# Kernel tuning notes

Measured on AMD Instinct MI355X. Metric: run time of the kernel, lower is better.

The kernel has to match this reference:

```python
import jax, jax.numpy as jnp
import numpy as np

N_NODES = 20000
N_EDGES = 320000
H = 4        # heads
C = 64       # channels per head
D = H * C    # 256, also input_dim
L = 4        # num_layers
NEG_SLOPE = 0.2


def setup_inputs() -> dict:
    key = jax.random.key(0)
    ks = jax.random.split(key, 8)
    x = jax.random.normal(ks[0], (N_NODES, D), jnp.float32)
    edge_index = jax.random.randint(ks[1], (2, N_EDGES), 0, N_NODES, dtype=jnp.int64)
    Ws = jax.random.normal(ks[2], (L, D, D), jnp.float32) * 0.05
    att_src = jax.random.normal(ks[3], (L, H, C), jnp.float32) * 0.05
    att_dst = jax.random.normal(ks[4], (L, H, C), jnp.float32) * 0.05
    biases = jax.random.normal(ks[5], (L, D), jnp.float32) * 0.05
    Wout = jax.random.normal(ks[6], (D, D), jnp.float32) * 0.05
    bout = jax.random.normal(ks[7], (D,), jnp.float32) * 0.05
    return {"x": x, "edge_index": edge_index, "Ws": Ws, "att_src": att_src,
            "att_dst": att_dst, "biases": biases, "Wout": Wout, "bout": bout}


def reference(x, edge_index, Ws, att_src, att_dst, biases, Wout, bout):
    n = x.shape[0]
    # PyG GATConv adds self-loops by default; same edge set each layer.
    loops = jnp.arange(n, dtype=edge_index.dtype)
    src = jnp.concatenate([edge_index[0], loops])  # message sources
    dst = jnp.concatenate([edge_index[1], loops])  # message targets (softmax groups)
    h = x
    for l in range(L):
        hp = (h @ Ws[l]).reshape(n, H, C)                      # [N,H,C]
        a_s = jnp.einsum('nhc,hc->nh', hp, att_src[l])          # [N,H]
        a_d = jnp.einsum('nhc,hc->nh', hp, att_dst[l])          # [N,H]
        e = jax.nn.leaky_relu(a_s[src] + a_d[dst], NEG_SLOPE)   # [E',H]
        # per-destination segment softmax (every node has a self-loop -> non-empty)
        m = jax.ops.segment_max(e, dst, num_segments=n)         # [N,H]
        ex = jnp.exp(e - m[dst])
        denom = jax.ops.segment_sum(ex, dst, num_segments=n)    # [N,H]
        alpha = ex / denom[dst]                                 # [E',H]
        msg = hp[src] * alpha[:, :, None]                       # [E',H,C]
        h = jax.ops.segment_sum(msg, dst, num_segments=n).reshape(n, D) + biases[l]
        h = jax.nn.elu(h)  # dropout is identity in eval mode
    g = jnp.mean(h, axis=0, keepdims=True)                      # mean pooling, single graph
    return g @ Wout + bout                                      # [1, D]
```

## Files before the change

### kernel.cpp

```cpp
#include <hip/hip_runtime.h>
#include <hip/hip_bf16.h>

#define H 4
#define C 64
#define D 256
#define NEG_SLOPE 0.2f
#define ESHIFT 8.0f

typedef _Float16 half_t;
typedef __attribute__((ext_vector_type(8))) _Float16 half8v;
typedef __attribute__((ext_vector_type(4))) float f32x4;


__device__ inline void fma_mix_pair(float& clo, float& chi, unsigned wu, float a) {
    asm("v_fma_mix_f32 %0, %2, %3, %0 op_sel_hi:[1,0,0]\n\t"
        "v_fma_mix_f32 %1, %2, %3, %1 op_sel:[1,0,0] op_sel_hi:[1,0,0]"
        : "+v"(clo), "+v"(chi)
        : "v"(wu), "v"(a));
}

__global__ void count_kernel(const int* __restrict__ ei, int E, int N, int* __restrict__ counts) {
    int i = blockIdx.x * blockDim.x + threadIdx.x;
    if (i >= E + N) return;
    int d = (i < E) ? ei[E + i] : (i - E);
    atomicAdd(&counts[d], 1);
}

__global__ __launch_bounds__(1024) void scan1(const int* __restrict__ counts,
                                              int* __restrict__ row_ptr,
                                              int* __restrict__ bsum, int N) {
    __shared__ int wsum[16];
    int tid = threadIdx.x, lane = tid & 63, wid = tid >> 6;
    int idx = blockIdx.x * 1024 + tid;
    int v = (idx < N) ? counts[idx] : 0;
    int val = v;
    #pragma unroll
    for (int o = 1; o < 64; o <<= 1) {
        int t = __shfl_up(val, o);
        if (lane >= o) val += t;
    }
    if (lane == 63) wsum[wid] = val;
    __syncthreads();
    int woff = 0;
    #pragma unroll
    for (int w = 0; w < 16; w++) woff += (w < wid) ? wsum[w] : 0;
    if (idx < N) row_ptr[idx] = woff + val - v;
    if (tid == 1023) bsum[blockIdx.x] = woff + val;
}

__global__ void scan2(int* __restrict__ bsum, int* __restrict__ row_ptr, int nb, int N) {
    int lane = threadIdx.x;
    int v = (lane < nb) ? bsum[lane] : 0;
    int val = v;
    #pragma unroll
    for (int o = 1; o < 64; o <<= 1) {
        int t = __shfl_up(val, o);
        if (lane >= o) val += t;
    }
    if (lane < nb) bsum[lane] = val - v;
    if (lane == 63) row_ptr[N] = val;
}

__global__ __launch_bounds__(1024) void scan3(int* __restrict__ row_ptr,
                                              const int* __restrict__ bsum,
                                              int* __restrict__ cursor, int N) {
    int idx = blockIdx.x * 1024 + threadIdx.x;
    if (idx >= N) return;
    int r = row_ptr[idx] + bsum[blockIdx.x];
    row_ptr[idx] = r;
    cursor[idx] = r;
}

__global__ void scatter_kernel(const int* __restrict__ ei, int E, int N,
                               int* __restrict__ cursor, int* __restrict__ csr_src) {
    int i = blockIdx.x * blockDim.x + threadIdx.x;
    if (i >= E + N) return;
    int s, d;
    if (i < E) { s = ei[i]; d = ei[E + i]; }
    else       { s = d = i - E; }
    int pos = atomicAdd(&cursor[d], 1);
    csr_src[pos] = s;
}

__global__ void conv_x(const float* __restrict__ in, half_t* __restrict__ xt, int total) {
    int t = blockIdx.x * blockDim.x + threadIdx.x;
    if (t >= total) return;
    int i = t >> 5, o = t & 31;
    const float* src = in + (size_t)i * 256 + o * 8;
    float4 v0 = *(const float4*)src;
    float4 v1 = *(const float4*)(src + 4);
    half_t q[8] __attribute__((aligned(16)));
    q[0] = (half_t)v0.x; q[1] = (half_t)v0.y; q[2] = (half_t)v0.z; q[3] = (half_t)v0.w;
    q[4] = (half_t)v1.x; q[5] = (half_t)v1.y; q[6] = (half_t)v1.z; q[7] = (half_t)v1.w;
    size_t dst = (size_t)(i >> 4) * 4096 + (o >> 2) * 512 + (o & 3) * 128 + (i & 15) * 8;
    *(half8v*)(xt + dst) = *(half8v*)q;
}

__global__ void conv_w(const float* __restrict__ W, half_t* __restrict__ wt, int total) {
    int idx = blockIdx.x * blockDim.x + threadIdx.x;
    if (idx >= total) return;
    int Lr = idx & 63;
    int s  = (idx >> 6) & 7;
    int cb = (idx >> 9) & 3;
    int h  = (idx >> 11) & 3;
    int l  = idx >> 13;
    int col = h * 64 + cb * 16 + (Lr & 15);
    int k0  = 32 * s + (Lr >> 4) * 8;
    half_t q[8] __attribute__((aligned(16)));
    #pragma unroll
    for (int j = 0; j < 8; j++)
        q[j] = (half_t)W[(size_t)l * 65536 + (size_t)(k0 + j) * 256 + col];
    *(half8v*)(wt + (size_t)idx * 8) = *(half8v*)q;
}

__global__ __launch_bounds__(256) void gemm_f16(
    const half_t* __restrict__ At, const half_t* __restrict__ Wt,
    const float* __restrict__ asrc, const float* __restrict__ adst,
    half_t* __restrict__ hp, float* __restrict__ as_out, float* __restrict__ ad_out,
    int Npad) {
    __shared__ float sp[4][4][16], sd[4][4][16];
    int nwg = gridDim.x;
    int bq = nwg >> 3, br = nwg & 7;
    int xcd = blockIdx.x & 7, bidx = blockIdx.x >> 3;
    int swz = (xcd < br ? xcd * (bq + 1) : br * (bq + 1) + (xcd - br) * bq) + bidx;
    int cb = threadIdx.x >> 6, lane = threadIdx.x & 63;
    int h = swz & 3, pg = swz >> 2;
    int rlo = lane & 15, q = lane >> 4;
    const half_t* pb = Wt + (size_t)h * 16384 + (size_t)cb * 4096 + lane * 8;

    half8v B[8];
    #pragma unroll
    for (int s = 0; s < 8; s++) B[s] = *(const half8v*)(pb + s * 512);

    float av = asrc[h * 64 + cb * 16 + rlo];
    float dv = adst[h * 64 + cb * 16 + rlo];
    half_t* hph = hp + (size_t)h * Npad * 64;

    #pragma unroll
    for (int pp = 0; pp < 4; pp++) {
        int p = pg * 4 + pp;
        const half_t* pa = At + (size_t)p * 4096 + lane * 8;

        f32x4 acc = (f32x4){0.f, 0.f, 0.f, 0.f};
        half8v A0 = *(const half8v*)(pa);
        half8v A1;
        #pragma unroll
        for (int s = 0; s < 8; s += 2) {
            A1 = *(const half8v*)(pa + (s + 1) * 512);
            acc = __builtin_amdgcn_mfma_f32_16x16x32_f16(A0, B[s], acc, 0, 0, 0);
            if (s < 6) A0 = *(const half8v*)(pa + (s + 2) * 512);
            acc = __builtin_amdgcn_mfma_f32_16x16x32_f16(A1, B[s + 1], acc, 0, 0, 0);
        }

        int grow = p * 16 + q * 4;
        #pragma unroll
        for (int i = 0; i < 4; i++)
            hph[(size_t)(grow + i) * 64 + cb * 16 + rlo] = (half_t)acc[i];

        float ps[4], pd[4];
        #pragma unroll
        for (int i = 0; i < 4; i++) { ps[i] = acc[i] * av; pd[i] = acc[i] * dv; }
        #pragma unroll
        for (int mask = 1; mask <= 8; mask <<= 1) {
            #pragma unroll
            for (int i = 0; i < 4; i++) {
                ps[i] += __shfl_xor(ps[i], mask);
                pd[i] += __shfl_xor(pd[i], mask);
            }
        }
        if (rlo == 0) {
            #pragma unroll
            for (int i = 0; i < 4; i++) {
                sp[pp][cb][q * 4 + i] = ps[i];
                sd[pp][cb][q * 4 + i] = pd[i];
            }
        }
    }
    __syncthreads();
    if (threadIdx.x < 64) {
        int pp = threadIdx.x >> 4, r = threadIdx.x & 15;
        float s_ = sp[pp][0][r] + sp[pp][1][r] + sp[pp][2][r] + sp[pp][3][r];
        float d_ = sd[pp][0][r] + sd[pp][1][r] + sd[pp][2][r] + sd[pp][3][r];
        int grow = (pg * 4 + pp) * 16 + r;
        as_out[(size_t)grow * 4 + h] = s_;
        ad_out[(size_t)grow * 4 + h] = d_;
    }
}

#define AGG_BODY(g)                                                          \
    {                                                                        \
        int e_ = 2 * (g) + es;                                               \
        int s_ = __float_as_int(pk[wv][e_][0]);                              \
        float a_ = pk[wv][e_][4 + hh];                                       \
        const uint4 w_ = *(const uint4*)(hpb + (size_t)s_ * 64);             \
        asum += a_;                                                          \
        fma_mix_pair(c0, c1, w_.x, a_);                                      \
        fma_mix_pair(c2, c3, w_.y, a_);                                      \
        fma_mix_pair(c4, c5, w_.z, a_);                                      \
        fma_mix_pair(c6, c7, w_.w, a_);                                      \
    }

__global__ __launch_bounds__(256) void gat_aggregate(
    const half_t* __restrict__ hp, const float* __restrict__ as_, const float* __restrict__ ad_,
    const int* __restrict__ row_ptr, const int* __restrict__ csr_src,
    const float* __restrict__ bias, half_t* __restrict__ hnext, int N, int Npad) {
    __shared__ float pk[4][64][8];
    int wv = threadIdx.x >> 6, lane = threadIdx.x & 63;
    int d = blockIdx.x * 4 + wv;
    if (d >= N) return;
    int r0 = row_ptr[d], deg = row_ptr[d + 1] - r0;
    float4 adv = *(const float4*)&ad_[(size_t)d * 4];

    if (deg <= 64) {
        if (lane < deg) {
            int s = csr_src[r0 + lane];
            float4 as4 = *(const float4*)&as_[(size_t)s * 4];
            float e0 = as4.x + adv.x, e1 = as4.y + adv.y;
            float e2 = as4.z + adv.z, e3 = as4.w + adv.w;
            e0 = e0 > 0.f ? e0 : NEG_SLOPE * e0;
            e1 = e1 > 0.f ? e1 : NEG_SLOPE * e1;
            e2 = e2 > 0.f ? e2 : NEG_SLOPE * e2;
            e3 = e3 > 0.f ? e3 : NEG_SLOPE * e3;
            float4 ex;
            ex.x = __expf(e0 - ESHIFT);
            ex.y = __expf(e1 - ESHIFT);
            ex.z = __expf(e2 - ESHIFT);
            ex.w = __expf(e3 - ESHIFT);
            pk[wv][lane][0] = __int_as_float(s);
            *(float4*)&pk[wv][lane][4] = ex;
        }

        int hh = lane >> 4;
        int es = (lane >> 3) & 1;
        int chq = lane & 7;
        const half_t* hpb = hp + (size_t)hh * Npad * 64 + chq * 8;
        float c0 = 0.f, c1 = 0.f, c2 = 0.f, c3 = 0.f;
        float c4 = 0.f, c5 = 0.f, c6 = 0.f, c7 = 0.f;
        float asum = 0.f;
        int full = deg >> 1;
        int g = 0;
        for (; g + 8 <= full; g += 8) {
            AGG_BODY(g)     AGG_BODY(g + 1) AGG_BODY(g + 2) AGG_BODY(g + 3)
            AGG_BODY(g + 4) AGG_BODY(g + 5) AGG_BODY(g + 6) AGG_BODY(g + 7)
        }
        for (; g + 4 <= full; g += 4) {
            AGG_BODY(g) AGG_BODY(g + 1) AGG_BODY(g + 2) AGG_BODY(g + 3)
        }
        for (; g < full; g++) { AGG_BODY(g) }
        if ((deg & 1) && es == 0) {
            int e_ = deg - 1;
            int s_ = __float_as_int(pk[wv][e_][0]);
            float a_ = pk[wv][e_][4 + hh];
            const uint4 w_ = *(const uint4*)(hpb + (size_t)s_ * 64);
            asum += a_;
            fma_mix_pair(c0, c1, w_.x, a_);
            fma_mix_pair(c2, c3, w_.y, a_);
            fma_mix_pair(c4, c5, w_.z, a_);
            fma_mix_pair(c6, c7, w_.w, a_);
        }
        c0 += __shfl_xor(c0, 8); c1 += __shfl_xor(c1, 8);
        c2 += __shfl_xor(c2, 8); c3 += __shfl_xor(c3, 8);
        c4 += __shfl_xor(c4, 8); c5 += __shfl_xor(c5, 8);
        c6 += __shfl_xor(c6, 8); c7 += __shfl_xor(c7, 8);
        asum += __shfl_xor(asum, 8);
        if (!(lane & 8)) {
            float inv = 1.0f / asum;
            int o = hh * 8 + chq;
            const float* bp = bias + o * 8;
            float vv[8] = {c0, c1, c2, c3, c4, c5, c6, c7};
            half_t oh[8] __attribute__((aligned(16)));
            #pragma unroll
            for (int j = 0; j < 8; j++) {
                float v = vv[j] * inv + bp[j];
                v = v > 0.f ? v : (__expf(v) - 1.0f);
                oh[j] = (half_t)v;
            }
            size_t dst = (size_t)(d >> 4) * 4096 + (o >> 2) * 512 + (o & 3) * 128 + (d & 15) * 8;
            *(half8v*)(hnext + dst) = *(half8v*)oh;
        }
    } else {
        float advA[4] = {adv.x, adv.y, adv.z, adv.w};
        #pragma unroll
        for (int hh = 0; hh < 4; hh++) {
            float advh = advA[hh];
            float ssum = 0.f;
            for (int i = lane; i < deg; i += 64) {
                int s = csr_src[r0 + i];
                float e = as_[(size_t)s * 4 + hh] + advh;
                e = e > 0.f ? e : NEG_SLOPE * e;
                ssum += __expf(e - ESHIFT);
            }
            #pragma unroll
            for (int o = 32; o; o >>= 1) ssum += __shfl_xor(ssum, o);
            float inv = 1.0f / ssum;
            const half_t* hph = hp + (size_t)hh * Npad * 64;
            float acc = 0.f;
            for (int i = 0; i < deg; i++) {
                int s = csr_src[r0 + i];
                float e = as_[(size_t)s * 4 + hh] + advh;
                e = e > 0.f ? e : NEG_SLOPE * e;
                acc += __expf(e - ESHIFT) * (float)hph[(size_t)s * 64 + lane];
            }
            float v = acc * inv + bias[hh * 64 + lane];
            v = v > 0.f ? v : (__expf(v) - 1.0f);
            int c = hh * 64 + lane;
            size_t dst = (size_t)(d >> 4) * 4096 + (c >> 5) * 512 + ((c >> 3) & 3) * 128 + (d & 15) * 8 + (c & 7);
            hnext[dst] = (half_t)v;
        }
    }
}

__global__ __launch_bounds__(256) void col_sum_f16(const half_t* __restrict__ hin,
                                                   float* __restrict__ partial, int N, int rows_per_blk) {
    int c = threadIdx.x;
    int r0 = blockIdx.x * rows_per_blk;
    int r1 = min(r0 + rows_per_blk, N);
    int coff = (c >> 5) * 512 + ((c >> 3) & 3) * 128 + (c & 7);
    float acc = 0.f;
    for (int r = r0; r < r1; r++)
        acc += (float)hin[(size_t)(r >> 4) * 4096 + coff + (r & 15) * 8];
    partial[(size_t)blockIdx.x * 256 + c] = acc;
}

__global__ __launch_bounds__(256) void final_kernel(const float* __restrict__ partial,
                                                    const float* __restrict__ Wout,
                                                    const float* __restrict__ bout,
                                                    float* __restrict__ out, float invN, int nb) {
    __shared__ float gl[256];
    int j = threadIdx.x;
    float s = 0.f;
    for (int b = 0; b < nb; b++) s += partial[(size_t)b * 256 + j];
    gl[j] = s;
    __syncthreads();
    float acc = 0.f;
    for (int i = 0; i < 256; i++) acc += gl[i] * Wout[i * 256 + j];
    out[j] = acc * invN + bout[j];
}

extern "C" void kernel_launch(void* const* d_in, const int* in_sizes, int n_in,
                              void* d_out, int out_size, void* d_ws, size_t ws_size,
                              hipStream_t stream) {
    const float* x       = (const float*)d_in[0];
    const int*   ei      = (const int*)d_in[1];
    const float* Ws      = (const float*)d_in[2];
    const float* att_src = (const float*)d_in[3];
    const float* att_dst = (const float*)d_in[4];
    const float* biases  = (const float*)d_in[5];
    const float* Wout    = (const float*)d_in[6];
    const float* bout    = (const float*)d_in[7];
    float* out = (float*)d_out;

    int N = in_sizes[0] / D;
    int E = in_sizes[1] / 2;
    int L = in_sizes[2] / (D * D);
    int Etot = E + N;
    int Npad = (N + 63) & ~63;

    char* ws = (char*)d_ws;
    size_t off = 0;
    auto alloc = [&](size_t bytes) -> void* {
        void* p = ws + off;
        off = (off + bytes + 255) & ~(size_t)255;
        return p;
    };
    half_t* xt     = (half_t*)alloc((size_t)Npad * D * 2);
    half_t* hp     = (half_t*)alloc((size_t)Npad * D * 2);
    float* a_s     = (float*)alloc((size_t)Npad * H * 4);
    float* a_d     = (float*)alloc((size_t)Npad * H * 4);
    half_t* wt     = (half_t*)alloc((size_t)L * D * D * 2);
    int*   counts  = (int*)alloc((size_t)N * 4);
    int*   row_ptr = (int*)alloc((size_t)(N + 1) * 4);
    int*   cursor  = (int*)alloc((size_t)N * 4);
    int*   bsum    = (int*)alloc(64 * 4);
    int*   csr_src = (int*)alloc((size_t)Etot * 4);
    int rows_per_blk = 254;
    int nb_pool = (N + rows_per_blk - 1) / rows_per_blk;
    float* partial = (float*)alloc((size_t)nb_pool * 256 * 4);
    if (off > ws_size) return;

    int thr = 256;

    int xtot = N * 32;
    conv_x<<<(xtot + thr - 1) / thr, thr, 0, stream>>>(x, xt, xtot);
    int wtot = L * 4 * 4 * 8 * 64;
    conv_w<<<(wtot + thr - 1) / thr, thr, 0, stream>>>(Ws, wt, wtot);

    hipMemsetAsync(counts, 0, (size_t)N * 4, stream);
    count_kernel<<<(Etot + thr - 1) / thr, thr, 0, stream>>>(ei, E, N, counts);
    int nb_scan = (N + 1023) / 1024;
    scan1<<<nb_scan, 1024, 0, stream>>>(counts, row_ptr, bsum, N);
    scan2<<<1, 64, 0, stream>>>(bsum, row_ptr, nb_scan, N);
    scan3<<<nb_scan, 1024, 0, stream>>>(row_ptr, bsum, cursor, N);
    scatter_kernel<<<(Etot + thr - 1) / thr, thr, 0, stream>>>(ei, E, N, cursor, csr_src);

    int gemm_blocks = (Npad / 64) * 4;
    int agg_blocks = (N + 3) / 4;
    for (int l = 0; l < L; l++) {
        gemm_f16<<<gemm_blocks, 256, 0, stream>>>(
            xt, wt + (size_t)l * D * D,
            att_src + (size_t)l * H * C, att_dst + (size_t)l * H * C,
            hp, a_s, a_d, Npad);
        gat_aggregate<<<agg_blocks, 256, 0, stream>>>(
            hp, a_s, a_d, row_ptr, csr_src, biases + (size_t)l * D, xt, N, Npad);
    }

    col_sum_f16<<<nb_pool, thr, 0, stream>>>(xt, partial, N, rows_per_blk);
    final_kernel<<<1, thr, 0, stream>>>(partial, Wout, bout, out, 1.0f / (float)N, nb_pool);
}
```

Baseline: 272.1 us.

## Split GAT aggregation by head with four destination nodes per wave

The aggregation grid now runs head-major. Each block covers one head and 16 destinations, and each wave handles 4 destinations using 16 lanes apiece, instead of one destination per wave across all 4 heads. The aim is to keep each head's slice of hp resident in L2 while its blocks run, and to shrink shared-memory staging to a 48-edge per-node buffer. The high-degree fallback is rewritten as a single fused pass with packed half loads. In exchange, edge indices and logits are re-read once per head, and lanes within a wave can diverge when the four nodes have different degrees.

```diff
diff --git a/kernel.cpp b/kernel.cpp
--- a/kernel.cpp
+++ b/kernel.cpp
@@ -6,6 +6,7 @@
 #define D 256
 #define NEG_SLOPE 0.2f
 #define ESHIFT 8.0f
+#define AGGC 48
 
 typedef _Float16 half_t;
 typedef __attribute__((ext_vector_type(8))) _Float16 half8v;
@@ -190,8 +191,8 @@
 #define AGG_BODY(g)                                                          \
     {                                                                        \
         int e_ = 2 * (g) + es;                                               \
-        int s_ = __float_as_int(pk[wv][e_][0]);                              \
-        float a_ = pk[wv][e_][4 + hh];                                       \
+        int s_ = __float_as_int(pk[wv][nn][e_][0]);                          \
+        float a_ = pk[wv][nn][e_][1];                                        \
         const uint4 w_ = *(const uint4*)(hpb + (size_t)s_ * 64);             \
         asum += a_;                                                          \
         fma_mix_pair(c0, c1, w_.x, a_);                                      \
@@ -203,54 +204,47 @@
 __global__ __launch_bounds__(256) void gat_aggregate(
     const half_t* __restrict__ hp, const float* __restrict__ as_, const float* __restrict__ ad_,
     const int* __restrict__ row_ptr, const int* __restrict__ csr_src,
-    const float* __restrict__ bias, half_t* __restrict__ hnext, int N, int Npad) {
-    __shared__ float pk[4][64][8];
+    const float* __restrict__ bias, half_t* __restrict__ hnext,
+    int N, int Npad, int ngroups) {
+    __shared__ float pk[4][4][AGGC][2];
     int wv = threadIdx.x >> 6, lane = threadIdx.x & 63;
-    int d = blockIdx.x * 4 + wv;
+    int h = blockIdx.x / ngroups;
+    int db = (blockIdx.x % ngroups) * 16;
+    int nn = lane >> 4;
+    int d = db + wv * 4 + nn;
     if (d >= N) return;
     int r0 = row_ptr[d], deg = row_ptr[d + 1] - r0;
-    float4 adv = *(const float4*)&ad_[(size_t)d * 4];
-
-    if (deg <= 64) {
-        if (lane < deg) {
-            int s = csr_src[r0 + lane];
-            float4 as4 = *(const float4*)&as_[(size_t)s * 4];
-            float e0 = as4.x + adv.x, e1 = as4.y + adv.y;
-            float e2 = as4.z + adv.z, e3 = as4.w + adv.w;
-            e0 = e0 > 0.f ? e0 : NEG_SLOPE * e0;
-            e1 = e1 > 0.f ? e1 : NEG_SLOPE * e1;
-            e2 = e2 > 0.f ? e2 : NEG_SLOPE * e2;
-            e3 = e3 > 0.f ? e3 : NEG_SLOPE * e3;
-            float4 ex;
-            ex.x = __expf(e0 - ESHIFT);
-            ex.y = __expf(e1 - ESHIFT);
-            ex.z = __expf(e2 - ESHIFT);
-            ex.w = __expf(e3 - ESHIFT);
-            pk[wv][lane][0] = __int_as_float(s);
-            *(float4*)&pk[wv][lane][4] = ex;
-        }
-
-        int hh = lane >> 4;
-        int es = (lane >> 3) & 1;
-        int chq = lane & 7;
-        const half_t* hpb = hp + (size_t)hh * Npad * 64 + chq * 8;
+    float adv = ad_[(size_t)d * 4 + h];
+    const half_t* hph = hp + (size_t)h * Npad * 64;
+
+    if (deg <= AGGC) {
+        int le = lane & 15;
+        #pragma unroll
+        for (int k = 0; k < 3; k++) {
+            int e = k * 16 + le;
+            if (e < deg) {
+                int s = csr_src[r0 + e];
+                float ev = as_[(size_t)s * 4 + h] + adv;
+                ev = ev > 0.f ? ev : NEG_SLOPE * ev;
+                pk[wv][nn][e][0] = __int_as_float(s);
+                pk[wv][nn][e][1] = __expf(ev - ESHIFT);
+            }
+        }
+        int es = (lane >> 3) & 1, chq = lane & 7;
+        const half_t* hpb = hph + chq * 8;
         float c0 = 0.f, c1 = 0.f, c2 = 0.f, c3 = 0.f;
         float c4 = 0.f, c5 = 0.f, c6 = 0.f, c7 = 0.f;
         float asum = 0.f;
         int full = deg >> 1;
         int g = 0;
-        for (; g + 8 <= full; g += 8) {
-            AGG_BODY(g)     AGG_BODY(g + 1) AGG_BODY(g + 2) AGG_BODY(g + 3)
-            AGG_BODY(g + 4) AGG_BODY(g + 5) AGG_BODY(g + 6) AGG_BODY(g + 7)
-        }
         for (; g + 4 <= full; g += 4) {
             AGG_BODY(g) AGG_BODY(g + 1) AGG_BODY(g + 2) AGG_BODY(g + 3)
         }
         for (; g < full; g++) { AGG_BODY(g) }
         if ((deg & 1) && es == 0) {
             int e_ = deg - 1;
-            int s_ = __float_as_int(pk[wv][e_][0]);
-            float a_ = pk[wv][e_][4 + hh];
+            int s_ = __float_as_int(pk[wv][nn][e_][0]);
+            float a_ = pk[wv][nn][e_][1];
             const uint4 w_ = *(const uint4*)(hpb + (size_t)s_ * 64);
             asum += a_;
             fma_mix_pair(c0, c1, w_.x, a_);
@@ -263,10 +257,10 @@
         c4 += __shfl_xor(c4, 8); c5 += __shfl_xor(c5, 8);
         c6 += __shfl_xor(c6, 8); c7 += __shfl_xor(c7, 8);
         asum += __shfl_xor(asum, 8);
-        if (!(lane & 8)) {
+        if (es == 0) {
             float inv = 1.0f / asum;
-            int o = hh * 8 + chq;
-            const float* bp = bias + o * 8;
+            int o = h * 8 + chq;
+            const float* bp = bias + h * 64 + chq * 8;
             float vv[8] = {c0, c1, c2, c3, c4, c5, c6, c7};
             half_t oh[8] __attribute__((aligned(16)));
             #pragma unroll
@@ -279,34 +273,30 @@
             *(half8v*)(hnext + dst) = *(half8v*)oh;
         }
     } else {
-        float advA[4] = {adv.x, adv.y, adv.z, adv.w};
-        #pragma unroll
-        for (int hh = 0; hh < 4; hh++) {
-            float advh = advA[hh];
-            float ssum = 0.f;
-            for (int i = lane; i < deg; i += 64) {
-                int s = csr_src[r0 + i];
-                float e = as_[(size_t)s * 4 + hh] + advh;
-                e = e > 0.f ? e : NEG_SLOPE * e;
-                ssum += __expf(e - ESHIFT);
-            }
-            #pragma unroll
-            for (int o = 32; o; o >>= 1) ssum += __shfl_xor(ssum, o);
-            float inv = 1.0f / ssum;
-            const half_t* hph = hp + (size_t)hh * Npad * 64;
-            float acc = 0.f;
-            for (int i = 0; i < deg; i++) {
-                int s = csr_src[r0 + i];
-                float e = as_[(size_t)s * 4 + hh] + advh;
-                e = e > 0.f ? e : NEG_SLOPE * e;
-                acc += __expf(e - ESHIFT) * (float)hph[(size_t)s * 64 + lane];
-            }
-            float v = acc * inv + bias[hh * 64 + lane];
+        int lc = lane & 15;
+        float cA = 0.f, cB = 0.f, cC = 0.f, cD = 0.f, asum = 0.f;
+        for (int i = 0; i < deg; i++) {
+            int s = csr_src[r0 + i];
+            float ev = as_[(size_t)s * 4 + h] + adv;
+            ev = ev > 0.f ? ev : NEG_SLOPE * ev;
+            float a = __expf(ev - ESHIFT);
+            asum += a;
+            const uint2 w = *(const uint2*)(hph + (size_t)s * 64 + lc * 4);
+            fma_mix_pair(cA, cB, w.x, a);
+            fma_mix_pair(cC, cD, w.y, a);
+        }
+        float inv = 1.0f / asum;
+        int c = h * 64 + lc * 4;
+        float vv[4] = {cA, cB, cC, cD};
+        half_t oh[4] __attribute__((aligned(8)));
+        #pragma unroll
+        for (int j = 0; j < 4; j++) {
+            float v = vv[j] * inv + bias[c + j];
             v = v > 0.f ? v : (__expf(v) - 1.0f);
-            int c = hh * 64 + lane;
-            size_t dst = (size_t)(d >> 4) * 4096 + (c >> 5) * 512 + ((c >> 3) & 3) * 128 + (d & 15) * 8 + (c & 7);
-            hnext[dst] = (half_t)v;
-        }
+            oh[j] = (half_t)v;
+        }
+        size_t dst = (size_t)(d >> 4) * 4096 + (c >> 5) * 512 + ((c >> 3) & 3) * 128 + (d & 15) * 8 + (c & 7);
+        *(uint2*)(hnext + dst) = *(uint2*)oh;
     }
 }
 
@@ -394,14 +384,15 @@
     scatter_kernel<<<(Etot + thr - 1) / thr, thr, 0, stream>>>(ei, E, N, cursor, csr_src);
 
     int gemm_blocks = (Npad / 64) * 4;
-    int agg_blocks = (N + 3) / 4;
+    int ngroups = (N + 15) / 16;
+    int agg_blocks = 4 * ngroups;
     for (int l = 0; l < L; l++) {
         gemm_f16<<<gemm_blocks, 256, 0, stream>>>(
             xt, wt + (size_t)l * D * D,
             att_src + (size_t)l * H * C, att_dst + (size_t)l * H * C,
             hp, a_s, a_d, Npad);
         gat_aggregate<<<agg_blocks, 256, 0, stream>>>(
-            hp, a_s, a_d, row_ptr, csr_src, biases + (size_t)l * D, xt, N, Npad);
+            hp, a_s, a_d, row_ptr, csr_src, biases + (size_t)l * D, xt, N, Npad, ngroups);
     }
 
     col_sum_f16<<<nb_pool, thr, 0, stream>>>(xt, partial, N, rows_per_blk);
```

Result: faster. 264.8 us, median of 2 (-2.7%).
